# Optimization experiments

Hardware: AMD Instinct MI355X
Metric: run time of the kernel (lower is better)

Reference implementation:

```python
import jax, jax.numpy as jnp
import numpy as np

D_IN = 1024
D_OUT = 1024

def setup_inputs() -> dict:
    key = jax.random.key(0)
    ks = jax.random.split(key, 7)
    s = 1.0 / np.sqrt(D_IN)
    x = jax.random.normal(ks[0], (4, 2048, D_IN), dtype=jnp.float32)
    Wq = jax.random.uniform(ks[1], (D_IN, D_OUT), jnp.float32, -s, s)
    bq = jax.random.uniform(ks[2], (D_OUT,), jnp.float32, -s, s)
    Wk = jax.random.uniform(ks[3], (D_IN, D_OUT), jnp.float32, -s, s)
    bk = jax.random.uniform(ks[4], (D_OUT,), jnp.float32, -s, s)
    Wv = jax.random.uniform(ks[5], (D_IN, D_OUT), jnp.float32, -s, s)
    bv = jax.random.uniform(ks[6], (D_OUT,), jnp.float32, -s, s)
    return {"x": x, "Wq": Wq, "bq": bq, "Wk": Wk, "bk": bk, "Wv": Wv, "bv": bv}

def reference(x, Wq, bq, Wk, bk, Wv, bv):
    # q,k,v: [B, T, d_out]
    q = x @ Wq + bq
    k = x @ Wk + bk
    v = x @ Wv + bv
    T = x.shape[1]
    scale = 1.0 / jnp.sqrt(jnp.asarray(D_OUT, x.dtype))
    qk = jnp.einsum('btd,bsd->bts', q, k) * scale  # [B, T, T]
    causal = jnp.tril(jnp.ones((T, T), dtype=bool))
    qk = jnp.where(causal, qk, -jnp.inf)
    probs = jax.nn.softmax(qk, axis=-1)
    return jnp.einsum('bts,bsd->btd', probs, v)
```

## Files before the change

kernel.cpp:

```cpp
#include <hip/hip_runtime.h>
#include <cstdint>
#include <cmath>

#define D_MODEL 1024
#define SEQ 2048
#define BATCH 4

typedef short bf16x8 __attribute__((ext_vector_type(8)));
typedef float f32x4 __attribute__((ext_vector_type(4)));

__device__ __forceinline__ short f2bf(float f) {
  union { float f; unsigned int u; } v; v.f = f;
  unsigned int r = (v.u + 0x7FFFu + ((v.u >> 16) & 1u)) >> 16;
  return (short)r;
}

__device__ __forceinline__ float bf2f(short h) {
  union { unsigned int u; float f; } v;
  v.u = ((unsigned int)(unsigned short)h) << 16;
  return v.f;
}

__device__ __forceinline__ f32x4 mfma16(bf16x8 a, bf16x8 b, f32x4 c) {
  return __builtin_amdgcn_mfma_f32_16x16x32_bf16(a, b, c, 0, 0, 0);
}

__device__ __forceinline__ void load_lds16(const void* g, void* l) {
  __builtin_amdgcn_global_load_lds(
      (const __attribute__((address_space(1))) unsigned int*)g,
      (__attribute__((address_space(3))) unsigned int*)l, 16, 0, 0);
}

__global__ __launch_bounds__(256) void convert_x(const float* __restrict__ x,
                                                 short* __restrict__ xb) {
  int i = blockIdx.x * 256 + threadIdx.x;
  float4 f = ((const float4*)x)[i];
  short4 h;
  h.x = f2bf(f.x); h.y = f2bf(f.y); h.z = f2bf(f.z); h.w = f2bf(f.w);
  ((short4*)xb)[i] = h;
}

__global__ __launch_bounds__(256) void transpose_w(const float* __restrict__ Wq,
                                                   const float* __restrict__ Wk,
                                                   const float* __restrict__ Wv,
                                                   short* __restrict__ wt) {
  const int mat = blockIdx.z;
  const float* __restrict__ W = (mat == 0) ? Wq : (mat == 1) ? Wk : Wv;
  short* __restrict__ o = wt + (size_t)mat * (D_MODEL * D_MODEL);
  __shared__ float tile[32][33];
  const int k0 = blockIdx.x * 32, n0 = blockIdx.y * 32;
  const int lx = threadIdx.x & 31, ly = threadIdx.x >> 5;
#pragma unroll
  for (int i = 0; i < 4; ++i) {
    int r = ly + i * 8;
    tile[r][lx] = W[(size_t)(k0 + r) * D_MODEL + n0 + lx];
  }
  __syncthreads();
#pragma unroll
  for (int i = 0; i < 4; ++i) {
    int r = ly + i * 8;
    o[(size_t)(n0 + r) * D_MODEL + k0 + lx] = f2bf(tile[lx][r]);
  }
}

__global__ __launch_bounds__(512, 4) void qkv_gemm(
    const short* __restrict__ xb, const short* __restrict__ wt,
    const float* __restrict__ bq, const float* __restrict__ bk,
    const float* __restrict__ bv, short* __restrict__ qo,
    short* __restrict__ ko, short* __restrict__ vo) {
  const int m0 = blockIdx.x * 256;
  const int n0 = blockIdx.y * 128;
  const int mat = blockIdx.z;
  const short* __restrict__ w = wt + (size_t)mat * (D_MODEL * D_MODEL);
  const float* __restrict__ bias = (mat == 0) ? bq : (mat == 1) ? bk : bv;

  __shared__ short a_lds[2][256 * 32];
  __shared__ short b_lds[2][128 * 32];

  const int tid = threadIdx.x;
  const int wid = tid >> 6;
  const int lane = tid & 63;
  const int quad = lane >> 4;
  const int l16 = lane & 15;
  const int wm = (wid >> 1) * 64;
  const int wn = (wid & 1) * 64;
  const int key = (l16 >> 1) & 3;

  f32x4 acc[4][4] = {};

  auto stage = [&](int k0, int buf) {
#pragma unroll
    for (int h = 0; h < 2; ++h) {
      const int c = tid + h * 512;
      load_lds16(xb + (size_t)(m0 + (c >> 2)) * D_MODEL + k0 +
                     (((c & 3) ^ ((c >> 3) & 3)) << 3),
                 (char*)&a_lds[buf][c * 8]);
    }
    load_lds16(w + (size_t)(n0 + (tid >> 2)) * D_MODEL + k0 +
                   (((tid & 3) ^ ((tid >> 3) & 3)) << 3),
               (char*)&b_lds[buf][tid * 8]);
  };

  stage(0, 0);
  for (int k0 = 0; k0 < D_MODEL; k0 += 32) {
    const int buf = (k0 >> 5) & 1;
    __syncthreads();
    if (k0 + 32 < D_MODEL) stage(k0 + 32, buf ^ 1);
    const short* al = a_lds[buf];
    const short* bl = b_lds[buf];
    bf16x8 af[4], bfr[4];
#pragma unroll
    for (int i = 0; i < 4; ++i)
      af[i] = *(const bf16x8*)(al + (wm + i * 16 + l16) * 32 +
                               ((quad ^ key) << 3));
#pragma unroll
    for (int j = 0; j < 4; ++j)
      bfr[j] = *(const bf16x8*)(bl + (wn + j * 16 + l16) * 32 +
                                ((quad ^ key) << 3));
#pragma unroll
    for (int i = 0; i < 4; ++i)
#pragma unroll
      for (int j = 0; j < 4; ++j)
        acc[i][j] = mfma16(af[i], bfr[j], acc[i][j]);
  }
#pragma unroll
  for (int i = 0; i < 4; ++i) {
#pragma unroll
    for (int j = 0; j < 4; ++j) {
#pragma unroll
      for (int r = 0; r < 4; ++r) {
        const int mrow = m0 + wm + i * 16 + quad * 4 + r;
        const int ncol = n0 + wn + j * 16 + l16;
        const float val = acc[i][j][r] + bias[ncol];
        const short h = f2bf(val);
        if (mat == 2) {
          const int bb = mrow >> 11;
          const int t = mrow & 2047;
          vo[((size_t)bb * D_MODEL + ncol) * SEQ + t] = h;
        } else if (mat == 0) {
          qo[(size_t)mrow * D_MODEL + ncol] = h;
        } else {
          ko[(size_t)mrow * D_MODEL + ncol] = h;
        }
      }
    }
  }
}

__global__ __launch_bounds__(512, 4) void sgemm(const short* __restrict__ qb,
                                                const short* __restrict__ kb,
                                                short* __restrict__ S) {
  if ((blockIdx.x >> 1) > blockIdx.y) return;
  const int n0 = blockIdx.x * 128;
  const int m0 = blockIdx.y * 256;
  const int b = blockIdx.z;
  const short* __restrict__ qp = qb + (size_t)b * SEQ * D_MODEL;
  const short* __restrict__ kp = kb + (size_t)b * SEQ * D_MODEL;

  __shared__ short a_lds[2][256 * 32];
  __shared__ short b_lds[2][128 * 32];

  const int tid = threadIdx.x;
  const int wid = tid >> 6;
  const int lane = tid & 63;
  const int quad = lane >> 4;
  const int l16 = lane & 15;
  const int wm = (wid >> 1) * 64;
  const int wn = (wid & 1) * 64;
  const int key = (l16 >> 1) & 3;

  f32x4 acc[4][4] = {};

  auto stage = [&](int k0, int buf) {
#pragma unroll
    for (int h = 0; h < 2; ++h) {
      const int c = tid + h * 512;
      load_lds16(qp + (size_t)(m0 + (c >> 2)) * D_MODEL + k0 +
                     (((c & 3) ^ ((c >> 3) & 3)) << 3),
                 (char*)&a_lds[buf][c * 8]);
    }
    load_lds16(kp + (size_t)(n0 + (tid >> 2)) * D_MODEL + k0 +
                   (((tid & 3) ^ ((tid >> 3) & 3)) << 3),
               (char*)&b_lds[buf][tid * 8]);
  };

  stage(0, 0);
  for (int k0 = 0; k0 < D_MODEL; k0 += 32) {
    const int buf = (k0 >> 5) & 1;
    __syncthreads();
    if (k0 + 32 < D_MODEL) stage(k0 + 32, buf ^ 1);
    const short* al = a_lds[buf];
    const short* bl = b_lds[buf];
    bf16x8 af[4], bfr[4];
#pragma unroll
    for (int i = 0; i < 4; ++i)
      af[i] = *(const bf16x8*)(al + (wm + i * 16 + l16) * 32 +
                               ((quad ^ key) << 3));
#pragma unroll
    for (int j = 0; j < 4; ++j)
      bfr[j] = *(const bf16x8*)(bl + (wn + j * 16 + l16) * 32 +
                                ((quad ^ key) << 3));
#pragma unroll
    for (int i = 0; i < 4; ++i)
#pragma unroll
      for (int j = 0; j < 4; ++j)
        acc[i][j] = mfma16(af[i], bfr[j], acc[i][j]);
  }
#pragma unroll
  for (int i = 0; i < 4; ++i) {
#pragma unroll
    for (int j = 0; j < 4; ++j) {
#pragma unroll
      for (int r = 0; r < 4; ++r) {
        const int mrow = m0 + wm + i * 16 + quad * 4 + r;
        const int ncol = n0 + wn + j * 16 + l16;
        S[((size_t)b * SEQ + mrow) * SEQ + ncol] = f2bf(acc[i][j][r] * 0.03125f);
      }
    }
  }
}

__global__ __launch_bounds__(256) void softmax_rows(const short* __restrict__ S,
                                                    short* __restrict__ P) {
  const int row = blockIdx.x;
  const int t = row & (SEQ - 1);
  const int tid = threadIdx.x;
  const short* __restrict__ srow = S + (size_t)row * SEQ;
  short* __restrict__ prow = P + (size_t)row * SEQ;

  __shared__ float red[4];

  const int nrd = (t >> 8) + 1;
  float v[8];
#pragma unroll
  for (int i = 0; i < 8; ++i) {
    const int c = tid + i * 256;
    v[i] = (i < nrd) ? ((c <= t) ? bf2f(srow[c]) : -1e30f) : -1e30f;
  }
  float m = v[0];
#pragma unroll
  for (int i = 1; i < 8; ++i) m = fmaxf(m, v[i]);
#pragma unroll
  for (int o = 32; o; o >>= 1) m = fmaxf(m, __shfl_xor(m, o));
  if ((tid & 63) == 0) red[tid >> 6] = m;
  __syncthreads();
  m = fmaxf(fmaxf(red[0], red[1]), fmaxf(red[2], red[3]));

  float e[8];
  float s = 0.f;
#pragma unroll
  for (int i = 0; i < 8; ++i) {
    e[i] = __expf(v[i] - m);
    s += e[i];
  }
#pragma unroll
  for (int o = 32; o; o >>= 1) s += __shfl_xor(s, o);
  __syncthreads();
  if ((tid & 63) == 0) red[tid >> 6] = s;
  __syncthreads();
  s = red[0] + red[1] + red[2] + red[3];
  const float rinv = 1.0f / s;
  const int nwr = nrd;
#pragma unroll
  for (int i = 0; i < 8; ++i)
    if (i < nwr) prow[tid + i * 256] = f2bf(e[i] * rinv);
}

__global__ __launch_bounds__(256) void pvgemm(const short* __restrict__ P,
                                              const short* __restrict__ vtb,
                                              float* __restrict__ out) {
  const int n0 = blockIdx.x * 128;
  const int b = blockIdx.y;
  const int zp = blockIdx.z;
  const int m0 = ((zp < 8) ? (15 - zp) : (zp - 8)) * 128;
  const short* __restrict__ pp = P + (size_t)b * SEQ * SEQ;
  const short* __restrict__ vp = vtb + (size_t)b * D_MODEL * SEQ;
  const int kmax = m0 + 128;

  __shared__ short a_lds[2][128 * 64];
  __shared__ short b_lds[2][128 * 64];

  const int tid = threadIdx.x;
  const int wid = tid >> 6;
  const int lane = tid & 63;
  const int quad = lane >> 4;
  const int l16 = lane & 15;
  const int mw = (wid >> 1) * 64;
  const int nw = (wid & 1) * 64;
  const int sw = l16 & 7;
  const int r_local = wid * 8 + (lane >> 3);
  const int c_sw = ((lane & 7) ^ (lane >> 3)) * 8;

  f32x4 acc[4][4] = {};

  auto stage = [&](int k0, int buf) {
#pragma unroll
    for (int it = 0; it < 4; ++it) {
      load_lds16(pp + (size_t)(m0 + it * 32 + r_local) * SEQ + k0 + c_sw,
                 (char*)a_lds[buf] + it * 4096 + wid * 1024);
      load_lds16(vp + (size_t)(n0 + it * 32 + r_local) * SEQ + k0 + c_sw,
                 (char*)b_lds[buf] + it * 4096 + wid * 1024);
    }
  };

  stage(0, 0);
  for (int k0 = 0; k0 < kmax; k0 += 64) {
    const int buf = (k0 >> 6) & 1;
    __syncthreads();
    if (k0 + 64 < kmax) stage(k0 + 64, buf ^ 1);
    const short* al = a_lds[buf];
    const short* bl = b_lds[buf];
#pragma unroll
    for (int kt = 0; kt < 2; ++kt) {
      bf16x8 af[4], bfr[4];
#pragma unroll
      for (int i = 0; i < 4; ++i)
        af[i] = *(const bf16x8*)(al + (mw + i * 16 + l16) * 64 +
                                 ((kt * 4 + quad) ^ sw) * 8);
#pragma unroll
      for (int i = 0; i < 4; ++i)
        bfr[i] = *(const bf16x8*)(bl + (nw + i * 16 + l16) * 64 +
                                  ((kt * 4 + quad) ^ sw) * 8);
#pragma unroll
      for (int i = 0; i < 4; ++i)
#pragma unroll
        for (int j = 0; j < 4; ++j)
          acc[i][j] = mfma16(af[i], bfr[j], acc[i][j]);
    }
  }
#pragma unroll
  for (int i = 0; i < 4; ++i) {
#pragma unroll
    for (int j = 0; j < 4; ++j) {
#pragma unroll
      for (int r = 0; r < 4; ++r) {
        const int mrow = m0 + mw + i * 16 + quad * 4 + r;
        const int ncol = n0 + nw + j * 16 + l16;
        out[((size_t)b * SEQ + mrow) * D_MODEL + ncol] = acc[i][j][r];
      }
    }
  }
}

extern "C" void kernel_launch(void* const* d_in, const int* in_sizes, int n_in,
                              void* d_out, int out_size, void* d_ws, size_t ws_size,
                              hipStream_t stream) {
  (void)in_sizes; (void)n_in; (void)out_size; (void)ws_size;
  const float* x  = (const float*)d_in[0];
  const float* Wq = (const float*)d_in[1];
  const float* bq = (const float*)d_in[2];
  const float* Wk = (const float*)d_in[3];
  const float* bk = (const float*)d_in[4];
  const float* Wv = (const float*)d_in[5];
  const float* bv = (const float*)d_in[6];
  float* out = (float*)d_out;

  char* ws = (char*)d_ws;
  short* xb = (short*)(ws);
  short* wt = (short*)(ws + 16777216);
  short* qo = (short*)(ws + 23068672);
  short* ko = (short*)(ws + 39845888);
  short* vo = (short*)(ws + 56623104);
  short* S  = (short*)(ws + 73400320);
  short* P  = (short*)(ws);

  convert_x<<<dim3(8192), dim3(256), 0, stream>>>(x, xb);
  transpose_w<<<dim3(32, 32, 3), dim3(256), 0, stream>>>(Wq, Wk, Wv, wt);
  qkv_gemm<<<dim3(32, 8, 3), dim3(512), 0, stream>>>(xb, wt, bq, bk, bv, qo, ko, vo);
  sgemm<<<dim3(16, 8, BATCH), dim3(512), 0, stream>>>(qo, ko, S);
  softmax_rows<<<dim3(BATCH * SEQ), dim3(256), 0, stream>>>(S, P);
  pvgemm<<<dim3(8, BATCH, 16), dim3(256), 0, stream>>>(P, vo, out);
}
```

Measured before the change: 258.1 us.

## Merge prep kernels, shrink sgemm tiles, vectorize softmax, retile pvgemm K-step

Fuses the x conversion and weight transpose into one launch to save a kernel launch. The score GEMM now uses 128x128 tiles with 256 threads and skips blocks above the diagonal at a finer grain, which cuts wasted causal work. Softmax now loads and stores eight contiguous bf16 values per thread with a 16-byte access instead of strided scalars. The PV GEMM switches to a 32-wide K step with the XOR-swizzled layout used in sgemm, halving its LDS footprint and adding an occupancy hint, at the cost of more loop iterations and barriers.

```diff
diff --git a/kernel.cpp b/kernel.cpp
--- a/kernel.cpp
+++ b/kernel.cpp
@@ -31,35 +31,39 @@
       (__attribute__((address_space(3))) unsigned int*)l, 16, 0, 0);
 }
 
-__global__ __launch_bounds__(256) void convert_x(const float* __restrict__ x,
-                                                 short* __restrict__ xb) {
-  int i = blockIdx.x * 256 + threadIdx.x;
-  float4 f = ((const float4*)x)[i];
-  short4 h;
-  h.x = f2bf(f.x); h.y = f2bf(f.y); h.z = f2bf(f.z); h.w = f2bf(f.w);
-  ((short4*)xb)[i] = h;
-}
-
-__global__ __launch_bounds__(256) void transpose_w(const float* __restrict__ Wq,
-                                                   const float* __restrict__ Wk,
-                                                   const float* __restrict__ Wv,
-                                                   short* __restrict__ wt) {
-  const int mat = blockIdx.z;
+__global__ __launch_bounds__(256) void prep(const float* __restrict__ x,
+                                            const float* __restrict__ Wq,
+                                            const float* __restrict__ Wk,
+                                            const float* __restrict__ Wv,
+                                            short* __restrict__ xb,
+                                            short* __restrict__ wt) {
+  __shared__ float tile[32][33];
+  const int bid = blockIdx.x;
+  if (bid < 8192) {
+    int i = bid * 256 + threadIdx.x;
+    float4 f = ((const float4*)x)[i];
+    short4 h;
+    h.x = f2bf(f.x); h.y = f2bf(f.y); h.z = f2bf(f.z); h.w = f2bf(f.w);
+    ((short4*)xb)[i] = h;
+    return;
+  }
+  const int r = bid - 8192;
+  const int mat = r >> 10;
+  const int rem = r & 1023;
   const float* __restrict__ W = (mat == 0) ? Wq : (mat == 1) ? Wk : Wv;
   short* __restrict__ o = wt + (size_t)mat * (D_MODEL * D_MODEL);
-  __shared__ float tile[32][33];
-  const int k0 = blockIdx.x * 32, n0 = blockIdx.y * 32;
+  const int k0 = (rem & 31) * 32, n0 = (rem >> 5) * 32;
   const int lx = threadIdx.x & 31, ly = threadIdx.x >> 5;
 #pragma unroll
   for (int i = 0; i < 4; ++i) {
-    int r = ly + i * 8;
-    tile[r][lx] = W[(size_t)(k0 + r) * D_MODEL + n0 + lx];
+    int rr = ly + i * 8;
+    tile[rr][lx] = W[(size_t)(k0 + rr) * D_MODEL + n0 + lx];
   }
   __syncthreads();
 #pragma unroll
   for (int i = 0; i < 4; ++i) {
-    int r = ly + i * 8;
-    o[(size_t)(n0 + r) * D_MODEL + k0 + lx] = f2bf(tile[lx][r]);
+    int rr = ly + i * 8;
+    o[(size_t)(n0 + rr) * D_MODEL + k0 + lx] = f2bf(tile[lx][rr]);
   }
 }
 
@@ -147,17 +151,17 @@
   }
 }
 
-__global__ __launch_bounds__(512, 4) void sgemm(const short* __restrict__ qb,
+__global__ __launch_bounds__(256, 4) void sgemm(const short* __restrict__ qb,
                                                 const short* __restrict__ kb,
                                                 short* __restrict__ S) {
-  if ((blockIdx.x >> 1) > blockIdx.y) return;
+  if (blockIdx.x > blockIdx.y) return;
   const int n0 = blockIdx.x * 128;
-  const int m0 = blockIdx.y * 256;
+  const int m0 = blockIdx.y * 128;
   const int b = blockIdx.z;
   const short* __restrict__ qp = qb + (size_t)b * SEQ * D_MODEL;
   const short* __restrict__ kp = kb + (size_t)b * SEQ * D_MODEL;
 
-  __shared__ short a_lds[2][256 * 32];
+  __shared__ short a_lds[2][128 * 32];
   __shared__ short b_lds[2][128 * 32];
 
   const int tid = threadIdx.x;
@@ -174,14 +178,13 @@
   auto stage = [&](int k0, int buf) {
 #pragma unroll
     for (int h = 0; h < 2; ++h) {
-      const int c = tid + h * 512;
-      load_lds16(qp + (size_t)(m0 + (c >> 2)) * D_MODEL + k0 +
-                     (((c & 3) ^ ((c >> 3) & 3)) << 3),
+      const int c = tid + h * 256;
+      const int go = (((c & 3) ^ ((c >> 3) & 3)) << 3);
+      load_lds16(qp + (size_t)(m0 + (c >> 2)) * D_MODEL + k0 + go,
                  (char*)&a_lds[buf][c * 8]);
-    }
-    load_lds16(kp + (size_t)(n0 + (tid >> 2)) * D_MODEL + k0 +
-                   (((tid & 3) ^ ((tid >> 3) & 3)) << 3),
-               (char*)&b_lds[buf][tid * 8]);
+      load_lds16(kp + (size_t)(n0 + (c >> 2)) * D_MODEL + k0 + go,
+                 (char*)&b_lds[buf][c * 8]);
+    }
   };
 
   stage(0, 0);
@@ -231,12 +234,16 @@
   __shared__ float red[4];
 
   const int nrd = (t >> 8) + 1;
+  const bool act = tid < nrd * 32;
+  const int base = tid * 8;
+
+  bf16x8 raw = {};
+  if (act) raw = *(const bf16x8*)(srow + base);
   float v[8];
 #pragma unroll
-  for (int i = 0; i < 8; ++i) {
-    const int c = tid + i * 256;
-    v[i] = (i < nrd) ? ((c <= t) ? bf2f(srow[c]) : -1e30f) : -1e30f;
-  }
+  for (int i = 0; i < 8; ++i)
+    v[i] = (act && (base + i <= t)) ? bf2f(raw[i]) : -1e30f;
+
   float m = v[0];
 #pragma unroll
   for (int i = 1; i < 8; ++i) m = fmaxf(m, v[i]);
@@ -260,73 +267,73 @@
   __syncthreads();
   s = red[0] + red[1] + red[2] + red[3];
   const float rinv = 1.0f / s;
-  const int nwr = nrd;
-#pragma unroll
-  for (int i = 0; i < 8; ++i)
-    if (i < nwr) prow[tid + i * 256] = f2bf(e[i] * rinv);
-}
-
-__global__ __launch_bounds__(256) void pvgemm(const short* __restrict__ P,
-                                              const short* __restrict__ vtb,
-                                              float* __restrict__ out) {
+  if (act) {
+    bf16x8 o8;
+#pragma unroll
+    for (int i = 0; i < 8; ++i) o8[i] = f2bf(e[i] * rinv);
+    *(bf16x8*)(prow + base) = o8;
+  }
+}
+
+__global__ __launch_bounds__(256, 4) void pvgemm(const short* __restrict__ P,
+                                                 const short* __restrict__ vtb,
+                                                 float* __restrict__ out) {
   const int n0 = blockIdx.x * 128;
   const int b = blockIdx.y;
-  const int zp = blockIdx.z;
-  const int m0 = ((zp < 8) ? (15 - zp) : (zp - 8)) * 128;
+  const int z = blockIdx.z;
+  const int mt = (z < 8) ? (15 - z) : (z - 8);
+  const int m0 = mt * 128;
+  const int kmax = m0 + 128;
   const short* __restrict__ pp = P + (size_t)b * SEQ * SEQ;
   const short* __restrict__ vp = vtb + (size_t)b * D_MODEL * SEQ;
-  const int kmax = m0 + 128;
-
-  __shared__ short a_lds[2][128 * 64];
-  __shared__ short b_lds[2][128 * 64];
+
+  __shared__ short a_lds[2][128 * 32];
+  __shared__ short b_lds[2][128 * 32];
 
   const int tid = threadIdx.x;
   const int wid = tid >> 6;
   const int lane = tid & 63;
   const int quad = lane >> 4;
   const int l16 = lane & 15;
-  const int mw = (wid >> 1) * 64;
-  const int nw = (wid & 1) * 64;
-  const int sw = l16 & 7;
-  const int r_local = wid * 8 + (lane >> 3);
-  const int c_sw = ((lane & 7) ^ (lane >> 3)) * 8;
+  const int wm = (wid >> 1) * 64;
+  const int wn = (wid & 1) * 64;
+  const int key = (l16 >> 1) & 3;
 
   f32x4 acc[4][4] = {};
 
   auto stage = [&](int k0, int buf) {
 #pragma unroll
-    for (int it = 0; it < 4; ++it) {
-      load_lds16(pp + (size_t)(m0 + it * 32 + r_local) * SEQ + k0 + c_sw,
-                 (char*)a_lds[buf] + it * 4096 + wid * 1024);
-      load_lds16(vp + (size_t)(n0 + it * 32 + r_local) * SEQ + k0 + c_sw,
-                 (char*)b_lds[buf] + it * 4096 + wid * 1024);
+    for (int h = 0; h < 2; ++h) {
+      const int c = tid + h * 256;
+      const int go = (((c & 3) ^ ((c >> 3) & 3)) << 3);
+      load_lds16(pp + (size_t)(m0 + (c >> 2)) * SEQ + k0 + go,
+                 (char*)&a_lds[buf][c * 8]);
+      load_lds16(vp + (size_t)(n0 + (c >> 2)) * SEQ + k0 + go,
+                 (char*)&b_lds[buf][c * 8]);
     }
   };
 
   stage(0, 0);
-  for (int k0 = 0; k0 < kmax; k0 += 64) {
-    const int buf = (k0 >> 6) & 1;
+  for (int k0 = 0; k0 < kmax; k0 += 32) {
+    const int buf = (k0 >> 5) & 1;
     __syncthreads();
-    if (k0 + 64 < kmax) stage(k0 + 64, buf ^ 1);
+    if (k0 + 32 < kmax) stage(k0 + 32, buf ^ 1);
     const short* al = a_lds[buf];
     const short* bl = b_lds[buf];
-#pragma unroll
-    for (int kt = 0; kt < 2; ++kt) {
-      bf16x8 af[4], bfr[4];
-#pragma unroll
-      for (int i = 0; i < 4; ++i)
-        af[i] = *(const bf16x8*)(al + (mw + i * 16 + l16) * 64 +
-                                 ((kt * 4 + quad) ^ sw) * 8);
-#pragma unroll
-      for (int i = 0; i < 4; ++i)
-        bfr[i] = *(const bf16x8*)(bl + (nw + i * 16 + l16) * 64 +
-                                  ((kt * 4 + quad) ^ sw) * 8);
-#pragma unroll
-      for (int i = 0; i < 4; ++i)
-#pragma unroll
-        for (int j = 0; j < 4; ++j)
-          acc[i][j] = mfma16(af[i], bfr[j], acc[i][j]);
-    }
+    bf16x8 af[4], bfr[4];
+#pragma unroll
+    for (int i = 0; i < 4; ++i)
+      af[i] = *(const bf16x8*)(al + (wm + i * 16 + l16) * 32 +
+                               ((quad ^ key) << 3));
+#pragma unroll
+    for (int j = 0; j < 4; ++j)
+      bfr[j] = *(const bf16x8*)(bl + (wn + j * 16 + l16) * 32 +
+                                ((quad ^ key) << 3));
+#pragma unroll
+    for (int i = 0; i < 4; ++i)
+#pragma unroll
+      for (int j = 0; j < 4; ++j)
+        acc[i][j] = mfma16(af[i], bfr[j], acc[i][j]);
   }
 #pragma unroll
   for (int i = 0; i < 4; ++i) {
@@ -334,8 +341,8 @@
     for (int j = 0; j < 4; ++j) {
 #pragma unroll
       for (int r = 0; r < 4; ++r) {
-        const int mrow = m0 + mw + i * 16 + quad * 4 + r;
-        const int ncol = n0 + nw + j * 16 + l16;
+        const int mrow = m0 + wm + i * 16 + quad * 4 + r;
+        const int ncol = n0 + wn + j * 16 + l16;
         out[((size_t)b * SEQ + mrow) * D_MODEL + ncol] = acc[i][j][r];
       }
     }
@@ -364,10 +371,9 @@
   short* S  = (short*)(ws + 73400320);
   short* P  = (short*)(ws);
 
-  convert_x<<<dim3(8192), dim3(256), 0, stream>>>(x, xb);
-  transpose_w<<<dim3(32, 32, 3), dim3(256), 0, stream>>>(Wq, Wk, Wv, wt);
+  prep<<<dim3(11264), dim3(256), 0, stream>>>(x, Wq, Wk, Wv, xb, wt);
   qkv_gemm<<<dim3(32, 8, 3), dim3(512), 0, stream>>>(xb, wt, bq, bk, bv, qo, ko, vo);
-  sgemm<<<dim3(16, 8, BATCH), dim3(512), 0, stream>>>(qo, ko, S);
+  sgemm<<<dim3(16, 16, BATCH), dim3(256), 0, stream>>>(qo, ko, S);
   softmax_rows<<<dim3(BATCH * SEQ), dim3(256), 0, stream>>>(S, P);
   pvgemm<<<dim3(8, BATCH, 16), dim3(256), 0, stream>>>(P, vo, out);
 }
```

Result: slower. 265.7 us (+2.9%).
